# Performance work log

Measured on AMD Instinct MI355X. Metric: run time of the kernel, lower is better.

Reference implementation:

```python
import jax, jax.numpy as jnp
import numpy as np

RADIUS = 0.2
K = 32
H_RES = 480
W_RES = 640
DIM = 128
EPS = 1e-5  # BatchNorm2d default eps


def setup_inputs() -> dict:
    key = jax.random.key(0)
    k1, k2, k3 = jax.random.split(key, 3)
    B, N = 2, 4096
    xyzp = jax.random.normal(k1, (B, N, 4), jnp.float32)
    features = jax.random.normal(k2, (B, N, DIM), jnp.float32)
    Wm = jax.random.normal(k3, (2 * DIM + 9, DIM), jnp.float32) * 0.05
    b = jnp.zeros((DIM,), jnp.float32)
    gamma = jnp.ones((DIM,), jnp.float32)
    beta = jnp.zeros((DIM,), jnp.float32)
    return {"xyzp": xyzp, "features": features, "Wm": Wm, "b": b, "gamma": gamma, "beta": beta}


def _ball_query(xyz, radius, k):
    # pytorch3d-style ball query: first k point indices (in index order) within radius, pad -1
    B, N, _ = xyz.shape
    d2 = jnp.sum((xyz[:, :, None, :] - xyz[:, None, :, :]) ** 2, axis=-1)  # [B,N,N]
    mask = d2 < radius * radius
    keyv = jnp.where(mask, jnp.arange(N)[None, None, :], N)
    order = jnp.argsort(keyv, axis=-1)[:, :, :k]  # stable sort -> first indices within radius
    count = mask.sum(axis=-1)
    return jnp.where(jnp.arange(k)[None, None, :] < count[:, :, None], order, -1)


def _knn_gather(x, idx):
    # x: [B,N,C], idx: [B,N,K] -> [B,N,K,C]
    B, N, Kk = idx.shape
    flat = idx.reshape(B, N * Kk)
    return jnp.take_along_axis(x, flat[:, :, None], axis=1).reshape(B, N, Kk, x.shape[-1])


def reference(xyzp, features, Wm, b, gamma, beta):
    B, N, _ = xyzp.shape
    # detached xyz with z (time) zeroed, used only for neighbor search
    xyz = jax.lax.stop_gradient(xyzp[..., :3]).at[..., 2].set(0.0)
    idx = _ball_query(xyz, RADIUS, K)
    self_idx = jnp.broadcast_to(jnp.arange(N)[None, :, None], (B, N, K))
    idx = jnp.where(idx == -1, self_idx, idx)

    d = xyzp[:, :, None, :] - _knn_gather(xyzp, idx)  # [B,N,K,4]
    ts = d[..., 2:3]
    ts = jnp.where(ts == 0, jnp.float32(1e-6), ts)
    res = jnp.array([W_RES, H_RES], jnp.float32)
    speed = d[..., :2] / ts * res  # [B,N,K,2]
    mean_speed = jnp.broadcast_to(speed.mean(axis=(1, 2), keepdims=True), speed.shape)
    p = jnp.abs(d[..., 3:4])

    knn_f = _knn_gather(features, idx)  # [B,N,K,DIM]
    f0 = jnp.broadcast_to(features[:, :, None, :], (B, N, K, features.shape[-1]))
    f = jnp.concatenate([f0, knn_f, d, speed, p, mean_speed], axis=-1)  # [B,N,K,2*DIM+9]

    h = f @ Wm + b  # Linear
    # BatchNorm2d in training mode: per-channel stats over (B,N,K)
    mu = h.mean(axis=(0, 1, 2))
    var = h.var(axis=(0, 1, 2))
    h = (h - mu) / jnp.sqrt(var + EPS) * gamma + beta
    h = jax.nn.relu(h)
    return h.max(axis=-2)  # max over K neighbors -> [B,N,DIM]
```

## Files before the change

### kernel.cpp

```cpp
#include <hip/hip_runtime.h>
#include <math.h>

#define NB   2
#define NP   4096
#define KNN  32
#define DIMC 128
#define NROWS (NB*NP)
#define MTOT  (NB*NP*KNN)
#define MASKBLOCKS 512
#define EGBLOCKS   512
#define MAINBLOCKS (NROWS/8)

static constexpr float R2 = 0.04f;

__global__ __launch_bounds__(256) void kB(const float* __restrict__ xyzp,
                                          const float* __restrict__ feat,
                                          const float* __restrict__ Wm,
                                          int* __restrict__ idx,
                                          double* __restrict__ spart,
                                          float* __restrict__ e,
                                          float* __restrict__ g)
{
    __shared__ float smem[NP*2 + 16*KNN + 8];

    if (blockIdx.x < MASKBLOCKS) {
#pragma clang fp contract(off)
        float* xy     = smem;
        int*   idxrow = (int*)(smem + NP*2);
        float* swr    = smem + NP*2 + 16*KNN;

        const int t    = threadIdx.x;
        const int w    = t >> 6;
        const int lane = t & 63;
        const int b    = blockIdx.x >> 8;
        const int p0   = (blockIdx.x & 255) * 16;
        const float* xb = xyzp + (size_t)b*NP*4;

        for (int q = t; q < NP; q += 256) {
            const float4 v = *(const float4*)(xb + (size_t)q*4);
            xy[q*2 + 0] = v.x;
            xy[q*2 + 1] = v.y;
        }
        __syncthreads();

        const int pl0 = p0 + w*4;
        float xi[4], yi[4];
        #pragma unroll
        for (int p = 0; p < 4; ++p) { xi[p] = xy[(pl0+p)*2]; yi[p] = xy[(pl0+p)*2+1]; }

        unsigned long long wacc[4] = {0ULL,0ULL,0ULL,0ULL};
        for (int c = 0; c < NP/64; ++c) {
            const float2 q = *(const float2*)(xy + (size_t)(c*64 + lane)*2);
            #pragma unroll
            for (int p = 0; p < 4; ++p) {
                const float dx = xi[p] - q.x;
                const float dy = yi[p] - q.y;
                const float dx2 = dx*dx;
                const float dy2 = dy*dy;
                const unsigned long long m = __ballot((dx2 + dy2) < R2);
                if (lane == c) wacc[p] = m;
            }
        }

        #pragma unroll
        for (int p = 0; p < 4; ++p) {
            unsigned long long wd = wacc[p];
            const int cnt = __popcll(wd);
            int pre = cnt;
            #pragma unroll
            for (int off = 1; off < 64; off <<= 1) {
                const int tv = __shfl_up(pre, off);
                if (lane >= off) pre += tv;
            }
            const int total = __shfl(pre, 63);
            int slot = pre - cnt;
            unsigned long long ww = wd;
            while (ww != 0ULL && slot < KNN) {
                const int bpos = __builtin_ctzll(ww);
                idxrow[(w*4 + p)*KNN + slot] = lane*64 + bpos;
                ww &= ww - 1ULL;
                ++slot;
            }
            const int iself = pl0 + p;
            for (int kk = min(total, KNN) + lane; kk < KNN; kk += 64)
                idxrow[(w*4 + p)*KNN + kk] = iself;
        }
        __syncthreads();

        float sxa = 0.f, sya = 0.f;
        #pragma unroll
        for (int p = 0; p < 4; ++p) {
            const int pt = b*NP + pl0 + p;
            float sxv = 0.f, syv = 0.f;
            if (lane < KNN) {
                const int j = idxrow[(w*4 + p)*KNN + lane];
                idx[(size_t)pt*KNN + lane] = j;
                const float4 pj = *(const float4*)(xb + (size_t)j*4);
                const float4 pi = *(const float4*)(xyzp + (size_t)pt*4);
                const float dz = pi.z - pj.z;
                const float ts = (dz == 0.f) ? 1e-6f : dz;
                const float rts = __builtin_amdgcn_rcpf(ts);
                sxv = (pi.x - pj.x)*rts*640.f;
                syv = (pi.y - pj.y)*rts*480.f;
            }
            sxa += sxv; sya += syv;
        }
        #pragma unroll
        for (int off = 32; off > 0; off >>= 1) {
            sxa += __shfl_down(sxa, off);
            sya += __shfl_down(sya, off);
        }
        if (lane == 0) { swr[w*2] = sxa; swr[w*2+1] = sya; }
        __syncthreads();
        if (t == 0) {
            const double s0 = ((double)swr[0] + (double)swr[2]) + ((double)swr[4] + (double)swr[6]);
            const double s1 = ((double)swr[1] + (double)swr[3]) + ((double)swr[5] + (double)swr[7]);
            spart[(size_t)blockIdx.x*2 + 0] = s0;
            spart[(size_t)blockIdx.x*2 + 1] = s1;
        }
    } else {
        float (*sf)[DIMC] = (float (*)[DIMC])smem;
        const int row0 = (blockIdx.x - MASKBLOCKS) * 16;
        for (int t = threadIdx.x; t < 16*DIMC; t += 256)
            ((float*)sf)[t] = feat[(size_t)row0*DIMC + t];
        __syncthreads();
        const int c = threadIdx.x;
        const int isg = c >> 7, cc = c & 127;
        const float* wcol = Wm + (size_t)(isg ? 128 : 0)*DIMC + cc;
        float acc[16];
        #pragma unroll
        for (int r = 0; r < 16; ++r) acc[r] = 0.0f;
        for (int kk = 0; kk < DIMC; ++kk) {
            const float w = wcol[(size_t)kk*DIMC];
            #pragma unroll
            for (int r = 0; r < 16; ++r) acc[r] = fmaf(sf[r][kk], w, acc[r]);
        }
        float* dst = isg ? g : e;
        #pragma unroll
        for (int r = 0; r < 16; ++r) dst[(size_t)(row0 + r)*DIMC + cc] = acc[r];
    }
}

__global__ __launch_bounds__(256) void kD(const float* __restrict__ xyzp,
                                          const int* __restrict__ idx,
                                          const float* __restrict__ e,
                                          const float* __restrict__ g,
                                          const float* __restrict__ Wm,
                                          const float* __restrict__ bbias,
                                          const double* __restrict__ spart,
                                          float* __restrict__ hmaxA,
                                          float* __restrict__ hminA,
                                          float* __restrict__ stpartT)
{
    __shared__ float  geo[4][KNN][8];
    __shared__ double rsp[256][2];
    __shared__ float  msS[2];
    __shared__ float  l1[4][DIMC], l2[4][DIMC];

    const int t        = threadIdx.x;
    const int row_base = blockIdx.x * 8;
    const int b        = row_base >> 12;

    {
        const double* sp = spart + (size_t)b * 512;
        rsp[t][0] = sp[t*2];
        rsp[t][1] = sp[t*2 + 1];
        __syncthreads();
        for (int st = 128; st > 0; st >>= 1) {
            if (t < st) { rsp[t][0] += rsp[t+st][0]; rsp[t][1] += rsp[t+st][1]; }
            __syncthreads();
        }
        if (t == 0) {
            msS[0] = (float)(rsp[0][0] / (double)(NP*KNN));
            msS[1] = (float)(rsp[0][1] / (double)(NP*KNN));
        }
        __syncthreads();
    }

    const int w    = t >> 6;
    const int lane = t & 63;
    const int c0   = lane * 2;
    const float msx = msS[0], msy = msS[1];

    float w2a[7], w2b[7];
    #pragma unroll
    for (int r = 0; r < 7; ++r) {
        w2a[r] = Wm[(256 + r)*DIMC + c0];
        w2b[r] = Wm[(256 + r)*DIMC + c0 + 1];
    }
    const float cva = fmaf(msx, Wm[263*DIMC + c0],     fmaf(msy, Wm[264*DIMC + c0],     bbias[c0]));
    const float cvb = fmaf(msx, Wm[263*DIMC + c0 + 1], fmaf(msy, Wm[264*DIMC + c0 + 1], bbias[c0+1]));

    const float* gb = g + (size_t)b*NP*DIMC + c0;
    float s1a = 0.f, s1b = 0.f, s2a = 0.f, s2b = 0.f;

    for (int rr = 0; rr < 2; ++rr) {
        const int row = row_base + w*2 + rr;
        if (lane < KNN) {
            const int j = idx[(size_t)row*KNN + lane];
            const float4 pj = *(const float4*)(xyzp + ((size_t)b*NP + j)*4);
            const float4 pi = *(const float4*)(xyzp + (size_t)row*4);
            const float dx = pi.x - pj.x;
            const float dy = pi.y - pj.y;
            const float dz = pi.z - pj.z;
            const float dwv = pi.w - pj.w;
            const float ts  = (dz == 0.f) ? 1e-6f : dz;
            const float rts = __builtin_amdgcn_rcpf(ts);
            geo[w][lane][0] = dx;
            geo[w][lane][1] = dy;
            geo[w][lane][2] = dz;
            geo[w][lane][3] = dwv;
            geo[w][lane][4] = dx*rts*640.f;
            geo[w][lane][5] = dy*rts*480.f;
            geo[w][lane][6] = fabsf(dwv);
            geo[w][lane][7] = __int_as_float(j);
        }
        __syncthreads();

        const float2 ee = *(const float2*)(e + (size_t)row*DIMC + c0);
        float mxa = -INFINITY, mxb = -INFINITY, mna = INFINITY, mnb = INFINITY;
        #pragma unroll 4
        for (int k = 0; k < KNN; ++k) {
            const float4 g0 = *(const float4*)&geo[w][k][0];
            const float4 g1 = *(const float4*)&geo[w][k][4];
            const int j = __float_as_int(g1.w);
            const float2 gg = *(const float2*)(gb + (size_t)j*DIMC);
            float ha = ee.x + gg.x + cva;
            float hb = ee.y + gg.y + cvb;
            ha = fmaf(g0.x, w2a[0], ha); hb = fmaf(g0.x, w2b[0], hb);
            ha = fmaf(g0.y, w2a[1], ha); hb = fmaf(g0.y, w2b[1], hb);
            ha = fmaf(g0.z, w2a[2], ha); hb = fmaf(g0.z, w2b[2], hb);
            ha = fmaf(g0.w, w2a[3], ha); hb = fmaf(g0.w, w2b[3], hb);
            ha = fmaf(g1.x, w2a[4], ha); hb = fmaf(g1.x, w2b[4], hb);
            ha = fmaf(g1.y, w2a[5], ha); hb = fmaf(g1.y, w2b[5], hb);
            ha = fmaf(g1.z, w2a[6], ha); hb = fmaf(g1.z, w2b[6], hb);
            mxa = fmaxf(mxa, ha); mna = fminf(mna, ha);
            mxb = fmaxf(mxb, hb); mnb = fminf(mnb, hb);
            s1a += ha; s2a = fmaf(ha, ha, s2a);
            s1b += hb; s2b = fmaf(hb, hb, s2b);
        }
        *(float2*)(hmaxA + (size_t)row*DIMC + c0) = make_float2(mxa, mxb);
        *(float2*)(hminA + (size_t)row*DIMC + c0) = make_float2(mna, mnb);
        __syncthreads();
    }

    l1[w][c0] = s1a; l1[w][c0+1] = s1b;
    l2[w][c0] = s2a; l2[w][c0+1] = s2b;
    __syncthreads();
    if (t < DIMC) {
        const float v = ((l1[0][t] + l1[1][t]) + l1[2][t]) + l1[3][t];
        stpartT[(size_t)t*MAINBLOCKS + blockIdx.x] = v;
    } else {
        const int tc = t - DIMC;
        const float v = ((l2[0][tc] + l2[1][tc]) + l2[2][tc]) + l2[3][tc];
        stpartT[(size_t)t*MAINBLOCKS + blockIdx.x] = v;
    }
}

__global__ __launch_bounds__(256) void kE(const float* __restrict__ stpartT,
                                          const float* __restrict__ gamma,
                                          const float* __restrict__ beta,
                                          float* __restrict__ abuf,
                                          float* __restrict__ dbuf)
{
    const int c = blockIdx.x;
    const int t = threadIdx.x;
    double s1 = 0.0, s2 = 0.0;
    for (int q = t; q < MAINBLOCKS; q += 256) {
        s1 += (double)stpartT[(size_t)c*MAINBLOCKS + q];
        s2 += (double)stpartT[(size_t)(c + DIMC)*MAINBLOCKS + q];
    }
    __shared__ double r1[256], r2[256];
    r1[t] = s1; r2[t] = s2;
    __syncthreads();
    for (int st = 128; st > 0; st >>= 1) {
        if (t < st) { r1[t] += r1[t+st]; r2[t] += r2[t+st]; }
        __syncthreads();
    }
    if (t == 0) {
        const double M   = (double)MTOT;
        const double mu  = r1[0] / M;
        const double var = r2[0] / M - mu*mu;
        const double inv = 1.0 / sqrt(var + 1e-5);
        const float a = (float)((double)gamma[c] * inv);
        abuf[c] = a;
        dbuf[c] = beta[c] - (float)mu * a;
    }
}

__global__ __launch_bounds__(256) void kF(const float* __restrict__ hmaxA,
                                          const float* __restrict__ hminA,
                                          const float* __restrict__ abuf,
                                          const float* __restrict__ dbuf,
                                          float* __restrict__ out)
{
    const int gid = blockIdx.x*256 + threadIdx.x;
    const int row = gid >> 6;
    const int c0  = (gid & 63)*2;
    const size_t off = (size_t)row*DIMC + c0;
    const float2 mx = *(const float2*)(hmaxA + off);
    const float2 mn = *(const float2*)(hminA + off);
    const float a0 = abuf[c0],   a1 = abuf[c0+1];
    const float d0 = dbuf[c0],   d1 = dbuf[c0+1];
    const float h0 = (a0 >= 0.f) ? mx.x : mn.x;
    const float h1 = (a1 >= 0.f) ? mx.y : mn.y;
    float2 o;
    o.x = fmaxf(fmaf(h0, a0, d0), 0.0f);
    o.y = fmaxf(fmaf(h1, a1, d1), 0.0f);
    *(float2*)(out + off) = o;
}

extern "C" void kernel_launch(void* const* d_in, const int* in_sizes, int n_in,
                              void* d_out, int out_size, void* d_ws, size_t ws_size,
                              hipStream_t stream)
{
    const float* xyzp  = (const float*)d_in[0];
    const float* feat  = (const float*)d_in[1];
    const float* Wm    = (const float*)d_in[2];
    const float* bbias = (const float*)d_in[3];
    const float* gamma = (const float*)d_in[4];
    const float* beta  = (const float*)d_in[5];

    char* ws = (char*)d_ws;
    const size_t MB = 1u << 20;
    int*    idx     = (int*)   (ws + 0);
    float*  g       = (float*) (ws + 1*MB);
    float*  e       = (float*) (ws + 5*MB);
    float*  hmaxA   = (float*) (ws + 9*MB);
    float*  hminA   = (float*) (ws + 13*MB);
    double* spart   = (double*)(ws + 17*MB);
    float*  abuf    = (float*) (ws + 17*MB + 65536);
    float*  dbuf    = (float*) (ws + 17*MB + 65536 + 1024);
    float*  stpartT = (float*) (ws + 18*MB);

    kB <<<MASKBLOCKS + EGBLOCKS, 256, 0, stream>>>(xyzp, feat, Wm, idx, spart, e, g);
    kD <<<MAINBLOCKS, 256, 0, stream>>>(xyzp, idx, e, g, Wm, bbias, spart, hmaxA, hminA, stpartT);
    kE <<<DIMC, 256, 0, stream>>>(stpartT, gamma, beta, abuf, dbuf);
    kF <<<(NROWS*64)/256, 256, 0, stream>>>(hmaxA, hminA, abuf, dbuf, (float*)d_out);
}
```

Baseline: 58.47 us.

## Defer mean-speed term to stats kernel, tile feature GEMM, halve main blocks

Removes the per-block reduction of mean-speed partials from the main kernel by folding the per-batch constant mean-speed contribution into the BatchNorm statistics algebraically inside kE, which now outputs a per-batch shift. The feature projection in kB is rewritten as a register-tiled 4x4 GEMM with weights staged through shared memory. kD processes 16 rows per block and uses wave barriers instead of block barriers. This trades redundant reductions and global weight reads for a larger stats kernel and some extra shared memory.

```diff
diff --git a/kernel.cpp b/kernel.cpp
--- a/kernel.cpp
+++ b/kernel.cpp
@@ -9,7 +9,7 @@
 #define MTOT  (NB*NP*KNN)
 #define MASKBLOCKS 512
 #define EGBLOCKS   512
-#define MAINBLOCKS (NROWS/8)
+#define MAINBLOCKS (NROWS/16)
 
 static constexpr float R2 = 0.04f;
 
@@ -21,7 +21,7 @@
                                           float* __restrict__ e,
                                           float* __restrict__ g)
 {
-    __shared__ float smem[NP*2 + 16*KNN + 8];
+    __shared__ float smem[8712];
 
     if (blockIdx.x < MASKBLOCKS) {
 #pragma clang fp contract(off)
@@ -51,6 +51,7 @@
         unsigned long long wacc[4] = {0ULL,0ULL,0ULL,0ULL};
         for (int c = 0; c < NP/64; ++c) {
             const float2 q = *(const float2*)(xy + (size_t)(c*64 + lane)*2);
+            const bool keep = (lane == c);
             #pragma unroll
             for (int p = 0; p < 4; ++p) {
                 const float dx = xi[p] - q.x;
@@ -58,7 +59,7 @@
                 const float dx2 = dx*dx;
                 const float dy2 = dy*dy;
                 const unsigned long long m = __ballot((dx2 + dy2) < R2);
-                if (lane == c) wacc[p] = m;
+                if (keep) wacc[p] = m;
             }
         }
 
@@ -119,25 +120,63 @@
             spart[(size_t)blockIdx.x*2 + 1] = s1;
         }
     } else {
-        float (*sf)[DIMC] = (float (*)[DIMC])smem;
+        float* sf = smem;
+        float* wt = smem + 2048;
+        const int t    = threadIdx.x;
+        const int w    = t >> 6;
+        const int lane = t & 63;
+        const int r0   = w * 4;
         const int row0 = (blockIdx.x - MASKBLOCKS) * 16;
-        for (int t = threadIdx.x; t < 16*DIMC; t += 256)
-            ((float*)sf)[t] = feat[(size_t)row0*DIMC + t];
-        __syncthreads();
-        const int c = threadIdx.x;
-        const int isg = c >> 7, cc = c & 127;
-        const float* wcol = Wm + (size_t)(isg ? 128 : 0)*DIMC + cc;
-        float acc[16];
-        #pragma unroll
-        for (int r = 0; r < 16; ++r) acc[r] = 0.0f;
-        for (int kk = 0; kk < DIMC; ++kk) {
-            const float w = wcol[(size_t)kk*DIMC];
-            #pragma unroll
-            for (int r = 0; r < 16; ++r) acc[r] = fmaf(sf[r][kk], w, acc[r]);
-        }
-        float* dst = isg ? g : e;
-        #pragma unroll
-        for (int r = 0; r < 16; ++r) dst[(size_t)(row0 + r)*DIMC + cc] = acc[r];
+
+        for (int q = t; q < 16*DIMC; q += 256)
+            sf[q] = feat[(size_t)row0*DIMC + q];
+
+        float acc[4][4];
+        #pragma unroll
+        for (int i = 0; i < 4; ++i)
+            #pragma unroll
+            for (int ci = 0; ci < 4; ++ci) acc[i][ci] = 0.f;
+
+        for (int kb = 0; kb < 8; ++kb) {
+            __syncthreads();
+            #pragma unroll
+            for (int it = 0; it < 16; ++it) {
+                const int cc = t;
+                wt[it*256 + cc] = Wm[(size_t)((cc >> 7)*128 + kb*16 + it)*DIMC + (cc & 127)];
+            }
+            __syncthreads();
+            #pragma unroll
+            for (int kks = 0; kks < 4; ++kks) {
+                const int kk0 = kks*4;
+                float4 sfv[4];
+                #pragma unroll
+                for (int i = 0; i < 4; ++i)
+                    sfv[i] = *(const float4*)&sf[(r0 + i)*DIMC + kb*16 + kk0];
+                #pragma unroll
+                for (int j = 0; j < 4; ++j) {
+                    const float w0 = wt[(kk0+j)*256 + lane];
+                    const float w1 = wt[(kk0+j)*256 + lane + 64];
+                    const float w2v= wt[(kk0+j)*256 + lane + 128];
+                    const float w3 = wt[(kk0+j)*256 + lane + 192];
+                    #pragma unroll
+                    for (int i = 0; i < 4; ++i) {
+                        const float s = (j==0) ? sfv[i].x : (j==1) ? sfv[i].y : (j==2) ? sfv[i].z : sfv[i].w;
+                        acc[i][0] = fmaf(s, w0, acc[i][0]);
+                        acc[i][1] = fmaf(s, w1, acc[i][1]);
+                        acc[i][2] = fmaf(s, w2v, acc[i][2]);
+                        acc[i][3] = fmaf(s, w3, acc[i][3]);
+                    }
+                }
+            }
+        }
+        #pragma unroll
+        for (int i = 0; i < 4; ++i) {
+            const int row = row0 + r0 + i;
+            e[(size_t)row*DIMC + lane]      = acc[i][0];
+            e[(size_t)row*DIMC + lane + 64] = acc[i][1];
+            g[(size_t)row*DIMC + lane]      = acc[i][2];
+            g[(size_t)row*DIMC + lane + 64] = acc[i][3];
+        }
     }
 }
 
@@ -147,40 +186,19 @@
                                           const float* __restrict__ g,
                                           const float* __restrict__ Wm,
                                           const float* __restrict__ bbias,
-                                          const double* __restrict__ spart,
                                           float* __restrict__ hmaxA,
                                           float* __restrict__ hminA,
                                           float* __restrict__ stpartT)
 {
-    __shared__ float  geo[4][KNN][8];
-    __shared__ double rsp[256][2];
-    __shared__ float  msS[2];
-    __shared__ float  l1[4][DIMC], l2[4][DIMC];
+    __shared__ float geo[4][KNN][8];
+    __shared__ float l1[4][DIMC], l2[4][DIMC];
 
     const int t        = threadIdx.x;
-    const int row_base = blockIdx.x * 8;
+    const int w        = t >> 6;
+    const int lane     = t & 63;
+    const int c0       = lane * 2;
+    const int row_base = blockIdx.x * 16;
     const int b        = row_base >> 12;
-
-    {
-        const double* sp = spart + (size_t)b * 512;
-        rsp[t][0] = sp[t*2];
-        rsp[t][1] = sp[t*2 + 1];
-        __syncthreads();
-        for (int st = 128; st > 0; st >>= 1) {
-            if (t < st) { rsp[t][0] += rsp[t+st][0]; rsp[t][1] += rsp[t+st][1]; }
-            __syncthreads();
-        }
-        if (t == 0) {
-            msS[0] = (float)(rsp[0][0] / (double)(NP*KNN));
-            msS[1] = (float)(rsp[0][1] / (double)(NP*KNN));
-        }
-        __syncthreads();
-    }
-
-    const int w    = t >> 6;
-    const int lane = t & 63;
-    const int c0   = lane * 2;
-    const float msx = msS[0], msy = msS[1];
 
     float w2a[7], w2b[7];
     #pragma unroll
@@ -188,14 +206,14 @@
         w2a[r] = Wm[(256 + r)*DIMC + c0];
         w2b[r] = Wm[(256 + r)*DIMC + c0 + 1];
     }
-    const float cva = fmaf(msx, Wm[263*DIMC + c0],     fmaf(msy, Wm[264*DIMC + c0],     bbias[c0]));
-    const float cvb = fmaf(msx, Wm[263*DIMC + c0 + 1], fmaf(msy, Wm[264*DIMC + c0 + 1], bbias[c0+1]));
+    const float cva = bbias[c0];
+    const float cvb = bbias[c0 + 1];
 
     const float* gb = g + (size_t)b*NP*DIMC + c0;
     float s1a = 0.f, s1b = 0.f, s2a = 0.f, s2b = 0.f;
 
-    for (int rr = 0; rr < 2; ++rr) {
-        const int row = row_base + w*2 + rr;
+    for (int rr = 0; rr < 4; ++rr) {
+        const int row = row_base + w*4 + rr;
         if (lane < KNN) {
             const int j = idx[(size_t)row*KNN + lane];
             const float4 pj = *(const float4*)(xyzp + ((size_t)b*NP + j)*4);
@@ -215,7 +233,7 @@
             geo[w][lane][6] = fabsf(dwv);
             geo[w][lane][7] = __int_as_float(j);
         }
-        __syncthreads();
+        __builtin_amdgcn_wave_barrier();
 
         const float2 ee = *(const float2*)(e + (size_t)row*DIMC + c0);
         float mxa = -INFINITY, mxb = -INFINITY, mna = INFINITY, mnb = INFINITY;
@@ -241,7 +259,7 @@
         }
         *(float2*)(hmaxA + (size_t)row*DIMC + c0) = make_float2(mxa, mxb);
         *(float2*)(hminA + (size_t)row*DIMC + c0) = make_float2(mna, mnb);
-        __syncthreads();
+        __builtin_amdgcn_wave_barrier();
     }
 
     l1[w][c0] = s1a; l1[w][c0+1] = s1b;
@@ -258,50 +276,75 @@
 }
 
 __global__ __launch_bounds__(256) void kE(const float* __restrict__ stpartT,
+                                          const double* __restrict__ spart,
+                                          const float* __restrict__ Wm,
                                           const float* __restrict__ gamma,
                                           const float* __restrict__ beta,
                                           float* __restrict__ abuf,
-                                          float* __restrict__ dbuf)
-{
+                                          float* __restrict__ dbuf2)
+{
+    __shared__ double red[256][8];
     const int c = blockIdx.x;
     const int t = threadIdx.x;
-    double s1 = 0.0, s2 = 0.0;
-    for (int q = t; q < MAINBLOCKS; q += 256) {
-        s1 += (double)stpartT[(size_t)c*MAINBLOCKS + q];
-        s2 += (double)stpartT[(size_t)(c + DIMC)*MAINBLOCKS + q];
-    }
-    __shared__ double r1[256], r2[256];
-    r1[t] = s1; r2[t] = s2;
+
+    red[t][0] = spart[(size_t)t*2];
+    red[t][1] = spart[(size_t)t*2 + 1];
+    red[t][2] = spart[(size_t)(t+256)*2];
+    red[t][3] = spart[(size_t)(t+256)*2 + 1];
+    red[t][4] = (double)stpartT[(size_t)c*MAINBLOCKS + t];
+    red[t][5] = (double)stpartT[(size_t)c*MAINBLOCKS + 256 + t];
+    red[t][6] = (double)stpartT[(size_t)(c + DIMC)*MAINBLOCKS + t];
+    red[t][7] = (double)stpartT[(size_t)(c + DIMC)*MAINBLOCKS + 256 + t];
     __syncthreads();
     for (int st = 128; st > 0; st >>= 1) {
-        if (t < st) { r1[t] += r1[t+st]; r2[t] += r2[t+st]; }
+        if (t < st) {
+            #pragma unroll
+            for (int q = 0; q < 8; ++q) red[t][q] += red[t+st][q];
+        }
         __syncthreads();
     }
     if (t == 0) {
-        const double M   = (double)MTOT;
-        const double mu  = r1[0] / M;
-        const double var = r2[0] / M - mu*mu;
+        const double NKd = (double)(NP*KNN);
+        const float ms0x = (float)(red[0][0] / NKd);
+        const float ms0y = (float)(red[0][1] / NKd);
+        const float ms1x = (float)(red[0][2] / NKd);
+        const float ms1y = (float)(red[0][3] / NKd);
+        const float wx = Wm[263*DIMC + c];
+        const float wy = Wm[264*DIMC + c];
+        const double cb0 = (double)fmaf(ms0x, wx, ms0y*wy);
+        const double cb1 = (double)fmaf(ms1x, wx, ms1y*wy);
+        const double s1b0 = red[0][4], s1b1 = red[0][5];
+        const double s2b0 = red[0][6], s2b1 = red[0][7];
+        const double M  = (double)MTOT;
+        const double S1 = s1b0 + s1b1 + NKd*(cb0 + cb1);
+        const double S2 = (s2b0 + 2.0*cb0*s1b0 + NKd*cb0*cb0)
+                        + (s2b1 + 2.0*cb1*s1b1 + NKd*cb1*cb1);
+        const double mu  = S1 / M;
+        const double var = S2 / M - mu*mu;
         const double inv = 1.0 / sqrt(var + 1e-5);
-        const float a = (float)((double)gamma[c] * inv);
-        abuf[c] = a;
-        dbuf[c] = beta[c] - (float)mu * a;
+        const double a  = (double)gamma[c] * inv;
+        const double db = (double)beta[c] - mu*a;
+        abuf[c] = (float)a;
+        dbuf2[c]        = (float)(db + cb0*a);
+        dbuf2[DIMC + c] = (float)(db + cb1*a);
     }
 }
 
 __global__ __launch_bounds__(256) void kF(const float* __restrict__ hmaxA,
                                           const float* __restrict__ hminA,
                                           const float* __restrict__ abuf,
-                                          const float* __restrict__ dbuf,
+                                          const float* __restrict__ dbuf2,
                                           float* __restrict__ out)
 {
     const int gid = blockIdx.x*256 + threadIdx.x;
     const int row = gid >> 6;
     const int c0  = (gid & 63)*2;
+    const int b   = row >> 12;
     const size_t off = (size_t)row*DIMC + c0;
     const float2 mx = *(const float2*)(hmaxA + off);
     const float2 mn = *(const float2*)(hminA + off);
-    const float a0 = abuf[c0],   a1 = abuf[c0+1];
-    const float d0 = dbuf[c0],   d1 = dbuf[c0+1];
+    const float a0 = abuf[c0],  a1 = abuf[c0+1];
+    const float d0 = dbuf2[b*DIMC + c0], d1 = dbuf2[b*DIMC + c0 + 1];
     const float h0 = (a0 >= 0.f) ? mx.x : mn.x;
     const float h1 = (a1 >= 0.f) ? mx.y : mn.y;
     float2 o;
@@ -330,11 +373,11 @@
     float*  hminA   = (float*) (ws + 13*MB);
     double* spart   = (double*)(ws + 17*MB);
     float*  abuf    = (float*) (ws + 17*MB + 65536);
-    float*  dbuf    = (float*) (ws + 17*MB + 65536 + 1024);
+    float*  dbuf2   = (float*) (ws + 17*MB + 66560);
     float*  stpartT = (float*) (ws + 18*MB);
 
     kB <<<MASKBLOCKS + EGBLOCKS, 256, 0, stream>>>(xyzp, feat, Wm, idx, spart, e, g);
-    kD <<<MAINBLOCKS, 256, 0, stream>>>(xyzp, idx, e, g, Wm, bbias, spart, hmaxA, hminA, stpartT);
-    kE <<<DIMC, 256, 0, stream>>>(stpartT, gamma, beta, abuf, dbuf);
-    kF <<<(NROWS*64)/256, 256, 0, stream>>>(hmaxA, hminA, abuf, dbuf, (float*)d_out);
-}
+    kD <<<MAINBLOCKS, 256, 0, stream>>>(xyzp, idx, e, g, Wm, bbias, hmaxA, hminA, stpartT);
+    kE <<<DIMC, 256, 0, stream>>>(stpartT, spart, Wm, gamma, beta, abuf, dbuf2);
+    kF <<<(NROWS*64)/256, 256, 0, stream>>>(hmaxA, hminA, abuf, dbuf2, (float*)d_out);
+}
```

New measurement: 67.09 us. +14.7%, slower.
